# Kernel tuning notes

Hardware: AMD Instinct MI355X
Metric: run time of the kernel (lower is better)

The kernel has to match this reference:

```python
import jax, jax.numpy as jnp
import numpy as np

N_NODES = 100000
N_EDGES = 1600000
IN_CH, HID_CH, OUT_CH = 128, 64, 32


def setup_inputs() -> dict:
    key = jax.random.key(0)
    k0, k1, k2, k3 = jax.random.split(key, 4)
    x = jax.random.normal(k0, (N_NODES, IN_CH), dtype=jnp.float32)
    edge_index = jax.random.randint(k1, (2, N_EDGES), 0, N_NODES, dtype=jnp.int64)
    # Glorot-style scaling for the two GCNConv weight matrices
    W1 = jax.random.normal(k2, (IN_CH, HID_CH), dtype=jnp.float32) * (2.0 / (IN_CH + HID_CH)) ** 0.5
    b1 = jnp.zeros((HID_CH,), dtype=jnp.float32)
    W2 = jax.random.normal(k3, (HID_CH, OUT_CH), dtype=jnp.float32) * (2.0 / (HID_CH + OUT_CH)) ** 0.5
    b2 = jnp.zeros((OUT_CH,), dtype=jnp.float32)
    return {"x": x, "edge_index": edge_index, "W1": W1, "b1": b1, "W2": W2, "b2": b2}


def _gcn_norm(edge_index, num_nodes):
    """Add self-loops and compute symmetric normalization deg^{-1/2}[src]*deg^{-1/2}[dst]."""
    loops = jnp.arange(num_nodes, dtype=edge_index.dtype)
    src = jnp.concatenate([edge_index[0], loops])  # message sources
    dst = jnp.concatenate([edge_index[1], loops])  # message targets
    deg = jax.ops.segment_sum(jnp.ones_like(dst, dtype=jnp.float32), dst,
                              num_segments=num_nodes)
    dinv = jnp.where(deg > 0, jax.lax.rsqrt(deg), 0.0)
    norm = dinv[src] * dinv[dst]  # [E + N]
    return src, dst, norm


def _gcn_conv(x, W, b, src, dst, norm, num_nodes):
    h = x @ W                                   # linear transform first
    msg = h[src] * norm[:, None]                # gather + scale per edge
    out = jax.ops.segment_sum(msg, dst, num_segments=num_nodes)  # scatter-add
    return out + b


def reference(x, edge_index, W1, b1, W2, b2):
    n = x.shape[0]
    src, dst, norm = _gcn_norm(edge_index, n)
    h = _gcn_conv(x, W1, b1, src, dst, norm, n)
    h = jax.nn.relu(h)
    # dropout is identity in eval mode (training=False)
    out = _gcn_conv(h, W2, b2, src, dst, norm, n)
    return out
```

## Files before the change

kernel.cpp:

```cpp
#include <hip/hip_runtime.h>

constexpr int N  = 100000;
constexpr int E  = 1600000;
constexpr int IN = 128, HID = 64, OUTC = 32;

constexpr int SHIFT = 9;
constexpr int NPB   = 1 << SHIFT;
constexpr int NB    = (N + NPB - 1) / NPB;
constexpr int CAP   = 16384;
constexpr int PB    = 256;
constexpr int CHUNK = E / PB;
constexpr int HB    = 256;

__device__ __forceinline__ unsigned short f2bf(float f) {
    union { float f; unsigned int u; } v; v.f = f;
    unsigned int u = v.u;
    return (unsigned short)((u + 0x7fffu + ((u >> 16) & 1u)) >> 16);
}
__device__ __forceinline__ float blo(unsigned u) { return __uint_as_float(u << 16); }
__device__ __forceinline__ float bhi(unsigned u) { return __uint_as_float(u & 0xffff0000u); }

__global__ __launch_bounds__(256) void k_hist(const int* __restrict__ dst,
                                              int* __restrict__ gmat) {
    __shared__ int h[NB];
    for (int i = threadIdx.x; i < NB; i += 256) h[i] = 0;
    __syncthreads();
    const int tid = blockIdx.x * 256 + threadIdx.x, nt = HB * 256;
    for (int e = tid; e < E; e += nt) atomicAdd(&h[dst[e] >> SHIFT], 1);
    __syncthreads();
    for (int i = threadIdx.x; i < NB; i += 256)
        gmat[i * HB + blockIdx.x] = h[i];
}

__global__ void k_bscan(const int* __restrict__ gmat, int* __restrict__ base,
                        int* __restrict__ cursor) {
    __shared__ int sb[256];
    const int t = threadIdx.x;
    int v = 0;
    if (t < NB) {
        const int4* row = (const int4*)(gmat + t * HB);
        #pragma unroll 8
        for (int j = 0; j < HB / 4; ++j) {
            int4 a = row[j];
            v += (a.x + a.y) + (a.z + a.w);
        }
    }
    sb[t] = v; __syncthreads();
    for (int off = 1; off < 256; off <<= 1) {
        int x = (t >= off) ? sb[t - off] : 0;
        __syncthreads();
        sb[t] += x;
        __syncthreads();
    }
    if (t < NB) { int ex = sb[t] - v; base[t] = ex; cursor[t] = ex; }
    if (t == 0) base[NB] = E;
}

__global__ __launch_bounds__(256) void k_part(const int* __restrict__ src,
                                              const int* __restrict__ dst,
                                              int* __restrict__ cursor,
                                              unsigned* __restrict__ packed) {
    __shared__ int lh[NB], lb[NB], lc[NB];
    const int t = threadIdx.x;
    const int beg = blockIdx.x * CHUNK, end = beg + CHUNK;
    for (int i = t; i < NB; i += 256) lh[i] = 0;
    __syncthreads();
    for (int e = beg + t; e < end; e += 256) atomicAdd(&lh[dst[e] >> SHIFT], 1);
    __syncthreads();
    for (int i = t; i < NB; i += 256) {
        lb[i] = lh[i] ? atomicAdd(&cursor[i], lh[i]) : 0;
        lc[i] = 0;
    }
    __syncthreads();
    for (int e = beg + t; e < end; e += 256) {
        int d = dst[e], b = d >> SHIFT;
        int idx = atomicAdd(&lc[b], 1);
        packed[lb[b] + idx] = ((unsigned)(d & (NPB - 1)) << 17) | (unsigned)src[e];
    }
}

__global__ __launch_bounds__(512) void k_build(const int* __restrict__ bbase,
                                               unsigned* __restrict__ packed,
                                               int* __restrict__ offs,
                                               float* __restrict__ dinv) {
    __shared__ int cnt[NPB];
    __shared__ unsigned stage[CAP];
    const int t = threadIdx.x, b = blockIdx.x;
    const int base = bbase[b], cntE = bbase[b + 1] - base;
    const int node0 = b << SHIFT;
    cnt[t] = 0;
    __syncthreads();
    for (int i = t; i < cntE; i += 512) atomicAdd(&cnt[packed[base + i] >> 17], 1);
    __syncthreads();
    const int v = cnt[t];
    __syncthreads();
    for (int off = 1; off < NPB; off <<= 1) {
        int x = (t >= off) ? cnt[t - off] : 0;
        __syncthreads();
        cnt[t] += x;
        __syncthreads();
    }
    const int ex = cnt[t] - v;
    const int node = node0 + t;
    if (node < N) {
        offs[node] = base + ex;
        dinv[node] = rsqrtf((float)v + 1.0f);
    }
    if (node == N) offs[N] = E;
    __syncthreads();
    cnt[t] = ex;
    __syncthreads();
    for (int i = t; i < cntE; i += 512) {
        unsigned p = packed[base + i];
        int idx = atomicAdd(&cnt[p >> 17], 1);
        if (idx < CAP) stage[idx] = p & 0x1FFFFu;
    }
    __syncthreads();
    for (int i = t; i < cntE; i += 512)
        packed[base + i] = stage[i];
}

__global__ __launch_bounds__(256) void k_gemm1(const float* __restrict__ X,
                                               const float* __restrict__ W,
                                               const float* __restrict__ dinv,
                                               unsigned short* __restrict__ Hs) {
    constexpr int R  = 32;
    constexpr int XS = IN + 4;
    __shared__ float ws[IN * HID];
    __shared__ float xs[R * XS];
    const int t    = threadIdx.x;
    const int row0 = blockIdx.x * R;

    if (blockIdx.x == 0 && t < HID / 2)
        ((unsigned*)(Hs + (size_t)N * HID))[t] = 0u;

    for (int i = t; i < IN * HID / 4; i += 256)
        ((float4*)ws)[i] = ((const float4*)W)[i];
    for (int i = t; i < R * IN / 4; i += 256) {
        int r = i / (IN / 4), k4 = i % (IN / 4);
        *(float4*)&xs[r * XS + k4 * 4] =
            ((const float4*)(X + (size_t)(row0 + r) * IN))[k4];
    }
    __syncthreads();

    const int col0 = (t & 15) * 4;
    const int r0   = (t >> 4) * 2;
    float4 a0 = {0, 0, 0, 0}, a1 = {0, 0, 0, 0};
    for (int k = 0; k < IN; ++k) {
        float4 w = *(const float4*)&ws[k * HID + col0];
        float x0 = xs[r0 * XS + k];
        float x1 = xs[(r0 + 1) * XS + k];
        a0.x += x0 * w.x; a0.y += x0 * w.y; a0.z += x0 * w.z; a0.w += x0 * w.w;
        a1.x += x1 * w.x; a1.y += x1 * w.y; a1.z += x1 * w.z; a1.w += x1 * w.w;
    }
    const float d0 = dinv[row0 + r0];
    const float d1 = dinv[row0 + r0 + 1];
    ushort4 p0 = {f2bf(a0.x * d0), f2bf(a0.y * d0), f2bf(a0.z * d0), f2bf(a0.w * d0)};
    ushort4 p1 = {f2bf(a1.x * d1), f2bf(a1.y * d1), f2bf(a1.z * d1), f2bf(a1.w * d1)};
    *(ushort4*)(Hs + (size_t)(row0 + r0) * HID + col0)       = p0;
    *(ushort4*)(Hs + (size_t)(row0 + r0 + 1) * HID + col0)   = p1;
}

__global__ __launch_bounds__(256) void k_gather1f(const int* __restrict__ offs,
                                                  const int* __restrict__ csr,
                                                  const float* __restrict__ dinv,
                                                  const unsigned short* __restrict__ Hs,
                                                  const float* __restrict__ b1,
                                                  const float* __restrict__ W2,
                                                  unsigned* __restrict__ H2u) {
    __shared__ float w2s[HID * OUTC];
    __shared__ int   sidx[4][2][96];
    __shared__ float wrow[4][2][64];
    const int t = threadIdx.x;
    if (blockIdx.x == 0 && t < OUTC / 2) H2u[(size_t)N * 16 + t] = 0u;
    for (int i = t; i < HID * OUTC / 4; i += 256)
        ((float4*)w2s)[i] = ((const float4*)W2)[i];
    __syncthreads();

    const int wave = t >> 6, lane = t & 63, half = lane >> 5, c2 = lane & 31;
    const int nA = blockIdx.x * 8 + wave * 2;
    const int myNode = nA + half;
    const int o0 = offs[myNode], o1 = offs[myNode + 1];
    const int deg  = o1 - o0;
    const int rdeg = (deg + 7) & ~7;
    for (int i = c2; i < deg; i += 32) sidx[wave][half][i] = csr[o0 + i];
    if (c2 < rdeg - deg) sidx[wave][half][deg + c2] = N;

    const unsigned* __restrict__ Hu = (const unsigned*)Hs;
    const float dn = dinv[myNode];
    unsigned su = Hu[(size_t)myNode * 32 + c2];
    float ax0 = blo(su), ay0 = bhi(su);
    float ax1 = 0, ay1 = 0, ax2 = 0, ay2 = 0, ax3 = 0, ay3 = 0;
    float ax4 = 0, ay4 = 0, ax5 = 0, ay5 = 0, ax6 = 0, ay6 = 0, ax7 = 0, ay7 = 0;
    for (int k = 0; k < rdeg; k += 8) {
        int4 sa = *(const int4*)&sidx[wave][half][k];
        int4 sb = *(const int4*)&sidx[wave][half][k + 4];
        unsigned u0 = Hu[(size_t)sa.x * 32 + c2];
        unsigned u1 = Hu[(size_t)sa.y * 32 + c2];
        unsigned u2 = Hu[(size_t)sa.z * 32 + c2];
        unsigned u3 = Hu[(size_t)sa.w * 32 + c2];
        unsigned u4 = Hu[(size_t)sb.x * 32 + c2];
        unsigned u5 = Hu[(size_t)sb.y * 32 + c2];
        unsigned u6 = Hu[(size_t)sb.z * 32 + c2];
        unsigned u7 = Hu[(size_t)sb.w * 32 + c2];
        ax0 += blo(u0);  ay0 += bhi(u0);
        ax1 += blo(u1);  ay1 += bhi(u1);
        ax2 += blo(u2);  ay2 += bhi(u2);
        ax3 += blo(u3);  ay3 += bhi(u3);
        ax4 += blo(u4);  ay4 += bhi(u4);
        ax5 += blo(u5);  ay5 += bhi(u5);
        ax6 += blo(u6);  ay6 += bhi(u6);
        ax7 += blo(u7);  ay7 += bhi(u7);
    }
    float sx = ((ax0 + ax1) + (ax2 + ax3)) + ((ax4 + ax5) + (ax6 + ax7));
    float sy = ((ay0 + ay1) + (ay2 + ay3)) + ((ay4 + ay5) + (ay6 + ay7));
    float2 bb = *(const float2*)(b1 + 2 * c2);
    wrow[wave][half][2 * c2]     = fmaxf(sx * dn + bb.x, 0.0f);
    wrow[wave][half][2 * c2 + 1] = fmaxf(sy * dn + bb.y, 0.0f);

    float acc = 0.0f;
    #pragma unroll 16
    for (int k = 0; k < HID; ++k)
        acc += wrow[wave][half][k] * w2s[k * OUTC + c2];
    float hv = acc * dn;
    float hv1 = __shfl_down(hv, 1, 64);
    if ((c2 & 1) == 0)
        H2u[(size_t)myNode * 16 + (c2 >> 1)] =
            (unsigned)f2bf(hv) | ((unsigned)f2bf(hv1) << 16);
}

__global__ __launch_bounds__(256) void k_gather2(const int* __restrict__ offs,
                                                 const int* __restrict__ csr,
                                                 const float* __restrict__ dinv,
                                                 const unsigned* __restrict__ H2u,
                                                 const float* __restrict__ b2,
                                                 float* __restrict__ out) {
    __shared__ int sidx[4][4][96];
    const int t = threadIdx.x;
    const int wave = t >> 6, lane = t & 63, q = lane >> 4, c2 = lane & 15;
    const int n0 = blockIdx.x * 16 + wave * 4;
    const int myNode = n0 + q;
    const int o0 = offs[myNode], o1 = offs[myNode + 1];
    const int deg  = o1 - o0;
    const int rdeg = (deg + 7) & ~7;
    for (int i = c2; i < deg; i += 16) sidx[wave][q][i] = csr[o0 + i];
    if (c2 < rdeg - deg) sidx[wave][q][deg + c2] = N;

    const float dn = dinv[myNode];
    unsigned su = H2u[(size_t)myNode * 16 + c2];
    float ax0 = blo(su), ay0 = bhi(su);
    float ax1 = 0, ay1 = 0, ax2 = 0, ay2 = 0, ax3 = 0, ay3 = 0;
    float ax4 = 0, ay4 = 0, ax5 = 0, ay5 = 0, ax6 = 0, ay6 = 0, ax7 = 0, ay7 = 0;
    for (int k = 0; k < rdeg; k += 8) {
        int4 sa = *(const int4*)&sidx[wave][q][k];
        int4 sb = *(const int4*)&sidx[wave][q][k + 4];
        unsigned u0 = H2u[(size_t)sa.x * 16 + c2];
        unsigned u1 = H2u[(size_t)sa.y * 16 + c2];
        unsigned u2 = H2u[(size_t)sa.z * 16 + c2];
        unsigned u3 = H2u[(size_t)sa.w * 16 + c2];
        unsigned u4 = H2u[(size_t)sb.x * 16 + c2];
        unsigned u5 = H2u[(size_t)sb.y * 16 + c2];
        unsigned u6 = H2u[(size_t)sb.z * 16 + c2];
        unsigned u7 = H2u[(size_t)sb.w * 16 + c2];
        ax0 += blo(u0);  ay0 += bhi(u0);
        ax1 += blo(u1);  ay1 += bhi(u1);
        ax2 += blo(u2);  ay2 += bhi(u2);
        ax3 += blo(u3);  ay3 += bhi(u3);
        ax4 += blo(u4);  ay4 += bhi(u4);
        ax5 += blo(u5);  ay5 += bhi(u5);
        ax6 += blo(u6);  ay6 += bhi(u6);
        ax7 += blo(u7);  ay7 += bhi(u7);
    }
    float sx = ((ax0 + ax1) + (ax2 + ax3)) + ((ax4 + ax5) + (ax6 + ax7));
    float sy = ((ay0 + ay1) + (ay2 + ay3)) + ((ay4 + ay5) + (ay6 + ay7));
    float2 bb = *(const float2*)(b2 + 2 * c2);
    float2 r;
    r.x = sx * dn + bb.x;
    r.y = sy * dn + bb.y;
    *(float2*)(out + (size_t)myNode * OUTC + 2 * c2) = r;
}

extern "C" void kernel_launch(void* const* d_in, const int* in_sizes, int n_in,
                              void* d_out, int out_size, void* d_ws, size_t ws_size,
                              hipStream_t stream) {
    const float* x   = (const float*)d_in[0];
    const int*   ei  = (const int*)d_in[1];
    const float* W1  = (const float*)d_in[2];
    const float* b1  = (const float*)d_in[3];
    const float* W2  = (const float*)d_in[4];
    const float* b2  = (const float*)d_in[5];
    float*       out = (float*)d_out;

    const int* srcp = ei;
    const int* dstp = ei + E;

    char* ws = (char*)d_ws;
    int*            bbase  = (int*)(ws + 4096);
    int*            cursor = (int*)(ws + 8192);
    int*            offs   = (int*)(ws + 16384);
    float*          dinv   = (float*)(ws + (512u << 10));
    unsigned*       packed = (unsigned*)(ws + (1u << 20));
    unsigned short* Hs     = (unsigned short*)(ws + (8u << 20));
    unsigned*       H2u    = (unsigned*)(ws + (21u << 20));
    int*            csr    = (int*)packed;
    int*            gmat   = (int*)Hs;

    k_hist <<<HB, 256, 0, stream>>>(dstp, gmat);
    k_bscan<<<1, 256, 0, stream>>>(gmat, bbase, cursor);
    k_part <<<PB, 256, 0, stream>>>(srcp, dstp, cursor, packed);
    k_build<<<NB, 512, 0, stream>>>(bbase, packed, offs, dinv);

    k_gemm1   <<<N / 32, 256, 0, stream>>>(x, W1, dinv, Hs);
    k_gather1f<<<N / 8,  256, 0, stream>>>(offs, csr, dinv, Hs, b1, W2, H2u);
    k_gather2 <<<N / 16, 256, 0, stream>>>(offs, csr, dinv, H2u, b2, out);
}
```

Measured before the change: 239.1 us.

## Use split-bf16 MFMA for first GEMM and enlarge partition grid

Replaces the scalar FP32 shared-memory GEMM for X@W1 with a single-wavefront kernel that keeps accuracy near FP32 by splitting operands into high and low bf16 parts and issuing three bf16 MFMA products per k-step. Each wave loads its X rows and W fragments straight from global memory into registers, with no LDS. This removes FP32 FMA throughput from the cost, but every wave converts the whole of W, adds conversion ALU work and uses uncoalesced 2-byte stores. The partition kernel grid is also raised from 256 to 800 blocks, which makes each block's chunk of edges smaller.

```diff
diff --git a/kernel.cpp b/kernel.cpp
--- a/kernel.cpp
+++ b/kernel.cpp
@@ -8,9 +8,12 @@
 constexpr int NPB   = 1 << SHIFT;
 constexpr int NB    = (N + NPB - 1) / NPB;
 constexpr int CAP   = 16384;
-constexpr int PB    = 256;
+constexpr int PB    = 800;
 constexpr int CHUNK = E / PB;
 constexpr int HB    = 256;
+
+typedef __attribute__((ext_vector_type(8))) short bf16x8_t;
+typedef __attribute__((ext_vector_type(4))) float f32x4_t;
 
 __device__ __forceinline__ unsigned short f2bf(float f) {
     union { float f; unsigned int u; } v; v.f = f;
@@ -120,45 +123,73 @@
         packed[base + i] = stage[i];
 }
 
-__global__ __launch_bounds__(256) void k_gemm1(const float* __restrict__ X,
-                                               const float* __restrict__ W,
-                                               const float* __restrict__ dinv,
-                                               unsigned short* __restrict__ Hs) {
-    constexpr int R  = 32;
-    constexpr int XS = IN + 4;
-    __shared__ float ws[IN * HID];
-    __shared__ float xs[R * XS];
-    const int t    = threadIdx.x;
-    const int row0 = blockIdx.x * R;
-
-    if (blockIdx.x == 0 && t < HID / 2)
-        ((unsigned*)(Hs + (size_t)N * HID))[t] = 0u;
-
-    for (int i = t; i < IN * HID / 4; i += 256)
-        ((float4*)ws)[i] = ((const float4*)W)[i];
-    for (int i = t; i < R * IN / 4; i += 256) {
-        int r = i / (IN / 4), k4 = i % (IN / 4);
-        *(float4*)&xs[r * XS + k4 * 4] =
-            ((const float4*)(X + (size_t)(row0 + r) * IN))[k4];
-    }
-    __syncthreads();
-
-    const int col0 = (t & 15) * 4;
-    const int r0   = (t >> 4) * 2;
-    float4 a0 = {0, 0, 0, 0}, a1 = {0, 0, 0, 0};
-    for (int k = 0; k < IN; ++k) {
-        float4 w = *(const float4*)&ws[k * HID + col0];
-        float x0 = xs[r0 * XS + k];
-        float x1 = xs[(r0 + 1) * XS + k];
-        a0.x += x0 * w.x; a0.y += x0 * w.y; a0.z += x0 * w.z; a0.w += x0 * w.w;
-        a1.x += x1 * w.x; a1.y += x1 * w.y; a1.z += x1 * w.z; a1.w += x1 * w.w;
-    }
-    const float d0 = dinv[row0 + r0];
-    const float d1 = dinv[row0 + r0 + 1];
-    ushort4 p0 = {f2bf(a0.x * d0), f2bf(a0.y * d0), f2bf(a0.z * d0), f2bf(a0.w * d0)};
-    ushort4 p1 = {f2bf(a1.x * d1), f2bf(a1.y * d1), f2bf(a1.z * d1), f2bf(a1.w * d1)};
-    *(ushort4*)(Hs + (size_t)(row0 + r0) * HID + col0)       = p0;
-    *(ushort4*)(Hs + (size_t)(row0 + r0 + 1) * HID + col0)   = p1;
+__global__ __launch_bounds__(64) void k_gemm1(const float* __restrict__ X,
+                                              const float* __restrict__ W,
+                                              const float* __restrict__ dinv,
+                                              unsigned short* __restrict__ Hs) {
+    const int l    = threadIdx.x;
+    const int row0 = blockIdx.x * 16;
+    const int rlo  = l & 15, khi = l >> 4;
+
+    if (blockIdx.x == 0 && l < HID / 2)
+        ((unsigned*)(Hs + (size_t)N * HID))[l] = 0u;
+
+    const float* xrow = X + (size_t)(row0 + rlo) * IN + khi * 8;
+    float4 xa[4], xb[4];
+    #pragma unroll
+    for (int ks = 0; ks < 4; ++ks) {
+        xa[ks] = *(const float4*)(xrow + ks * 32);
+        xb[ks] = *(const float4*)(xrow + ks * 32 + 4);
+    }
+
+    bf16x8_t wh[4][4], wl[4][4];
+    #pragma unroll
+    for (int ks = 0; ks < 4; ++ks) {
+        #pragma unroll
+        for (int ct = 0; ct < 4; ++ct) {
+            const float* wp = W + (ks * 32 + khi * 8) * HID + ct * 16 + rlo;
+            #pragma unroll
+            for (int e = 0; e < 8; ++e) {
+                float w = wp[e * HID];
+                unsigned short h = f2bf(w);
+                float r = w - __uint_as_float((unsigned)h << 16);
+                wh[ks][ct][e] = (short)h;
+                wl[ks][ct][e] = (short)f2bf(r);
+            }
+        }
+    }
+
+    f32x4_t acc[4] = {{0,0,0,0},{0,0,0,0},{0,0,0,0},{0,0,0,0}};
+    #pragma unroll
+    for (int ks = 0; ks < 4; ++ks) {
+        float xr[8] = {xa[ks].x, xa[ks].y, xa[ks].z, xa[ks].w,
+                       xb[ks].x, xb[ks].y, xb[ks].z, xb[ks].w};
+        bf16x8_t ah, al;
+        #pragma unroll
+        for (int e = 0; e < 8; ++e) {
+            unsigned short h = f2bf(xr[e]);
+            ah[e] = (short)h;
+            al[e] = (short)f2bf(xr[e] - __uint_as_float((unsigned)h << 16));
+        }
+        #pragma unroll
+        for (int ct = 0; ct < 4; ++ct)
+            acc[ct] = __builtin_amdgcn_mfma_f32_16x16x32_bf16(ah, wh[ks][ct], acc[ct], 0, 0, 0);
+        #pragma unroll
+        for (int ct = 0; ct < 4; ++ct)
+            acc[ct] = __builtin_amdgcn_mfma_f32_16x16x32_bf16(al, wh[ks][ct], acc[ct], 0, 0, 0);
+        #pragma unroll
+        for (int ct = 0; ct < 4; ++ct)
+            acc[ct] = __builtin_amdgcn_mfma_f32_16x16x32_bf16(ah, wl[ks][ct], acc[ct], 0, 0, 0);
+    }
+
+    const int orow = row0 + khi * 4;
+    #pragma unroll
+    for (int r = 0; r < 4; ++r) {
+        const float d = dinv[orow + r];
+        #pragma unroll
+        for (int ct = 0; ct < 4; ++ct)
+            Hs[(size_t)(orow + r) * HID + ct * 16 + rlo] = f2bf(acc[ct][r] * d);
+    }
 }
 
 __global__ __launch_bounds__(256) void k_gather1f(const int* __restrict__ offs,
@@ -310,7 +341,7 @@
     k_part <<<PB, 256, 0, stream>>>(srcp, dstp, cursor, packed);
     k_build<<<NB, 512, 0, stream>>>(bbase, packed, offs, dinv);
 
-    k_gemm1   <<<N / 32, 256, 0, stream>>>(x, W1, dinv, Hs);
+    k_gemm1   <<<N / 16, 64,  0, stream>>>(x, W1, dinv, Hs);
     k_gather1f<<<N / 8,  256, 0, stream>>>(offs, csr, dinv, Hs, b1, W2, H2u);
     k_gather2 <<<N / 16, 256, 0, stream>>>(offs, csr, dinv, H2u, b2, out);
 }
```

Measured after the change: 232.3 us. 2.9% less time.
